# Kernel optimization log

Measured on AMD Instinct MI355X. Metric: run time of the kernel, lower is better.

The kernel has to match this reference:

```python
import jax, jax.numpy as jnp
import numpy as np

N_NODES = 100000
N_EDGES = 1600000
N_GRAPHS = 2000
F_IN = 64
HID = 64


def setup_inputs() -> dict:
    key = jax.random.key(0)
    ks = jax.random.split(key, 8)
    h = jax.random.normal(ks[0], (N_NODES, F_IN), jnp.float32)
    edge_src = jax.random.randint(ks[1], (N_EDGES,), 0, N_NODES, jnp.int32)
    edge_dst = jax.random.randint(ks[2], (N_EDGES,), 0, N_NODES, jnp.int32)
    graph_ids = jnp.sort(jax.random.randint(ks[3], (N_NODES,), 0, N_GRAPHS, jnp.int32))
    # GraphConv weights (glorot-ish scale) and biases, 3 layers 64->64
    sc = 1.0 / np.sqrt(F_IN)
    W0 = jax.random.normal(ks[4], (F_IN, HID), jnp.float32) * sc
    W1 = jax.random.normal(ks[5], (HID, HID), jnp.float32) * sc
    W2 = jax.random.normal(ks[6], (HID, HID), jnp.float32) * sc
    b0 = jnp.zeros((HID,), jnp.float32)
    b1 = jnp.zeros((HID,), jnp.float32)
    b2 = jnp.zeros((HID,), jnp.float32)
    return dict(h=h, edge_src=edge_src, edge_dst=edge_dst, graph_ids=graph_ids,
                W0=W0, b0=b0, W1=W1, b1=b1, W2=W2, b2=b2)


def _gcn_layer(h, W, b, src, dst, out_deg_isqrt, in_deg_isqrt, apply_relu):
    # DGL GraphConv, norm='both': D_in^{-1/2} A D_out^{-1/2} h W + b
    hw = (h * out_deg_isqrt[:, None]) @ W          # weight/norm commute with sum
    m = jax.ops.segment_sum(hw[src], dst, num_segments=N_NODES)  # gather->scatter-add
    m = m * in_deg_isqrt[:, None] + b
    return jax.nn.relu(m) if apply_relu else m


def reference(h, edge_src, edge_dst, graph_ids, W0, b0, W1, b1, W2, b2):
    ones = jnp.ones((N_EDGES,), h.dtype)
    out_deg = jnp.clip(jax.ops.segment_sum(ones, edge_src, num_segments=N_NODES), 1.0, None)
    in_deg = jnp.clip(jax.ops.segment_sum(ones, edge_dst, num_segments=N_NODES), 1.0, None)
    odi = jax.lax.rsqrt(out_deg)
    idi = jax.lax.rsqrt(in_deg)
    params = [(W0, b0), (W1, b1), (W2, b2)]
    for i, (W, b) in enumerate(params):
        h = _gcn_layer(h, W, b, edge_src, edge_dst, odi, idi, apply_relu=(i < len(params) - 1))
    # self.factor = sqrt(dim) / mean(||h||) computed as python float -> detached constant
    factor = jnp.sqrt(jnp.asarray(HID, h.dtype)) / jnp.mean(jnp.linalg.norm(h, axis=1))
    factor = jax.lax.stop_gradient(factor)
    h = h * factor
    # SumPooling over batched graphs
    return jax.ops.segment_sum(h, graph_ids, num_segments=N_GRAPHS)
```

## Files before the change

### kernel.cpp

```cpp
#include <hip/hip_runtime.h>
#include <hip/hip_fp16.h>

#define N_NODES 100000
#define N_EDGES 1600000
#define N_GRAPHS 2000
#define HID 64
#define NB 391
#define CH 4096
#define CAP 5120
#define GATHER_GRID 2048
#define GEMM_GRID 512
#define N_GROUPS (N_NODES / 4)
#define N_TILE16 (N_NODES / 16)

typedef _Float16 half8 __attribute__((ext_vector_type(8)));
typedef float f32x4 __attribute__((ext_vector_type(4)));

__global__ __launch_bounds__(256) void k_zero_i32(int* __restrict__ p, int n) {
    int i = blockIdx.x * 256 + threadIdx.x;
    if (i < n) p[i] = 0;
}

__global__ __launch_bounds__(256) void k_partition_dual(const int* __restrict__ src, const int* __restrict__ dst,
                                                        int* __restrict__ gcur_dst, int* __restrict__ gcur_src,
                                                        unsigned* __restrict__ part_dst,
                                                        unsigned char* __restrict__ part_src) {
    __shared__ unsigned stage[CH];
    __shared__ int lcnt[NB];
    __shared__ int lexcl[NB];
    __shared__ int lofs[NB];
    __shared__ int runbase[NB];
    __shared__ int scanbuf[512];
    int tid = threadIdx.x;
    int e0 = blockIdx.x * CH;
    int n = min(CH, N_EDGES - e0);

    int sv[16], dv[16];
#pragma unroll
    for (int k = 0; k < 16; ++k) {
        int i = k * 256 + tid;
        if (i < n) { sv[k] = src[e0 + i]; dv[k] = dst[e0 + i]; }
        else dv[k] = -1;
    }

    for (int i = tid; i < NB; i += 256) lcnt[i] = 0;
    __syncthreads();
#pragma unroll
    for (int k = 0; k < 16; ++k)
        if (dv[k] >= 0) atomicAdd(&lcnt[dv[k] >> 8], 1);
    __syncthreads();
    for (int s = tid; s < 512; s += 256) scanbuf[s] = (s < NB) ? lcnt[s] : 0;
    __syncthreads();
    for (int off = 1; off < 512; off <<= 1) {
        int i0 = tid, i1 = tid + 256;
        int v0 = scanbuf[i0] + ((i0 >= off) ? scanbuf[i0 - off] : 0);
        int v1 = scanbuf[i1] + ((i1 >= off) ? scanbuf[i1 - off] : 0);
        __syncthreads();
        scanbuf[i0] = v0;
        scanbuf[i1] = v1;
        __syncthreads();
    }
    for (int i = tid; i < NB; i += 256) {
        int ex = scanbuf[i] - lcnt[i];
        lexcl[i] = ex;
        lofs[i] = ex;
    }
    __syncthreads();
#pragma unroll
    for (int k = 0; k < 16; ++k) {
        if (dv[k] >= 0) {
            int p = atomicAdd(&lofs[dv[k] >> 8], 1);
            stage[p] = ((unsigned)sv[k] << 8) | (unsigned)(dv[k] & 255);
        }
    }
    __syncthreads();
    for (int b = tid; b < NB; b += 256)
        if (lcnt[b]) runbase[b] = atomicAdd(&gcur_dst[b], lcnt[b]);
    __syncthreads();
    for (int i = tid; i < n; i += 256) {
        int lo = 0, hi = NB - 1;
        while (lo < hi) {
            int mid = (lo + hi + 1) >> 1;
            if (lexcl[mid] <= i) lo = mid; else hi = mid - 1;
        }
        int pos = runbase[lo] + (i - lexcl[lo]);
        if (pos < CAP) part_dst[(size_t)lo * CAP + pos] = stage[i];
    }
    __syncthreads();

    for (int i = tid; i < NB; i += 256) lcnt[i] = 0;
    __syncthreads();
#pragma unroll
    for (int k = 0; k < 16; ++k)
        if (dv[k] >= 0) atomicAdd(&lcnt[sv[k] >> 8], 1);
    __syncthreads();
    for (int s = tid; s < 512; s += 256) scanbuf[s] = (s < NB) ? lcnt[s] : 0;
    __syncthreads();
    for (int off = 1; off < 512; off <<= 1) {
        int i0 = tid, i1 = tid + 256;
        int v0 = scanbuf[i0] + ((i0 >= off) ? scanbuf[i0 - off] : 0);
        int v1 = scanbuf[i1] + ((i1 >= off) ? scanbuf[i1 - off] : 0);
        __syncthreads();
        scanbuf[i0] = v0;
        scanbuf[i1] = v1;
        __syncthreads();
    }
    for (int i = tid; i < NB; i += 256) {
        int ex = scanbuf[i] - lcnt[i];
        lexcl[i] = ex;
        lofs[i] = ex;
    }
    __syncthreads();
    unsigned char* stage8 = (unsigned char*)stage;
#pragma unroll
    for (int k = 0; k < 16; ++k) {
        if (dv[k] >= 0) {
            int p = atomicAdd(&lofs[sv[k] >> 8], 1);
            stage8[p] = (unsigned char)(sv[k] & 255);
        }
    }
    __syncthreads();
    for (int b = tid; b < NB; b += 256)
        if (lcnt[b]) runbase[b] = atomicAdd(&gcur_src[b], lcnt[b]);
    __syncthreads();
    for (int i = tid; i < n; i += 256) {
        int lo = 0, hi = NB - 1;
        while (lo < hi) {
            int mid = (lo + hi + 1) >> 1;
            if (lexcl[mid] <= i) lo = mid; else hi = mid - 1;
        }
        int pos = runbase[lo] + (i - lexcl[lo]);
        if (pos < CAP) part_src[(size_t)lo * CAP + pos] = stage8[i];
    }
}

__global__ __launch_bounds__(512) void k_scan_buckets(const int* __restrict__ gcur_dst,
                                                      int* __restrict__ bucket_base) {
    __shared__ int sd[512];
    int tid = threadIdx.x;
    int v = (tid < NB) ? gcur_dst[tid] : 0;
    sd[tid] = v;
    __syncthreads();
    for (int off = 1; off < 512; off <<= 1) {
        int t = (tid >= off) ? sd[tid - off] : 0;
        __syncthreads();
        sd[tid] += t;
        __syncthreads();
    }
    if (tid < NB) bucket_base[tid] = sd[tid] - v;
    if (tid == 0) bucket_base[NB] = sd[NB - 1];
}

__global__ __launch_bounds__(256) void k_csr(const unsigned* __restrict__ part_dst,
                                             const int* __restrict__ bucket_base,
                                             int* __restrict__ rowbeg, int* __restrict__ rowend,
                                             float* __restrict__ idi, int* __restrict__ col) {
    __shared__ int cnt[256];
    __shared__ int cur[256];
    __shared__ int wsum[4];
    int b = blockIdx.x;
    int tid = threadIdx.x;
    int base = bucket_base[b];
    int nE = bucket_base[b + 1] - base;
    const unsigned* pb = part_dst + (size_t)b * CAP;
    cnt[tid] = 0;
    __syncthreads();
    for (int i = tid; i < nE; i += 256) atomicAdd(&cnt[pb[i] & 255], 1);
    __syncthreads();
    int c = cnt[tid];
    int incl = c;
#pragma unroll
    for (int off = 1; off < 64; off <<= 1) {
        int t = __shfl_up(incl, off, 64);
        if ((tid & 63) >= off) incl += t;
    }
    if ((tid & 63) == 63) wsum[tid >> 6] = incl;
    __syncthreads();
    int add = 0;
    for (int w = 0; w < (tid >> 6); ++w) add += wsum[w];
    incl += add;
    int excl = incl - c;
    int v = b * 256 + tid;
    if (v < N_NODES) {
        rowbeg[v] = base + excl;
        rowend[v] = base + incl;
        idi[v] = rsqrtf((float)max(c, 1));
    }
    cur[tid] = excl;
    __syncthreads();
    for (int i = tid; i < nE; i += 256) {
        unsigned e = pb[i];
        int p = atomicAdd(&cur[e & 255], 1);
        col[base + p] = (int)(e >> 8);
    }
}

__global__ __launch_bounds__(256) void k_count(const unsigned char* __restrict__ part_src,
                                               const int* __restrict__ gcur_src,
                                               float* __restrict__ odi) {
    __shared__ int cnt[256];
    int b = blockIdx.x;
    int tid = threadIdx.x;
    int nE = gcur_src[b];
    const unsigned char* pb = part_src + (size_t)b * CAP;
    cnt[tid] = 0;
    __syncthreads();
    for (int i = tid; i < nE; i += 256) atomicAdd(&cnt[pb[i]], 1);
    __syncthreads();
    int v = b * 256 + tid;
    if (v < N_NODES) odi[v] = rsqrtf((float)max(cnt[tid], 1));
}

template <int F32IN>
__global__ __launch_bounds__(256) void k_gemm_mfma(const void* __restrict__ inv,
                                                   const float* __restrict__ W,
                                                   const float* __restrict__ odi,
                                                   __half* __restrict__ zs) {
    __shared__ _Float16 Wt[64 * 64];
    int tid = threadIdx.x;
    for (int i = tid; i < 4096; i += 256) {
        int k = i >> 6, j = i & 63;
        Wt[j * 64 + k] = (_Float16)W[i];
    }
    __syncthreads();

    int lane = tid & 63;
    int wid = tid >> 6;
    int lrow = lane & 15;
    int lgrp = lane >> 4;

    half8 Bf[4][2];
#pragma unroll
    for (int nt = 0; nt < 4; ++nt)
#pragma unroll
        for (int kh = 0; kh < 2; ++kh)
            Bf[nt][kh] = *(half8*)&Wt[(nt * 16 + lrow) * 64 + kh * 32 + lgrp * 8];

    for (int t = blockIdx.x * 4 + wid; t < N_TILE16; t += GEMM_GRID * 4) {
        int v0 = t * 16;
        half8 a0, a1;
        if (F32IN) {
            const float* A = (const float*)inv + (size_t)(v0 + lrow) * 64 + lgrp * 8;
            float4 f0 = *(const float4*)A;
            float4 f1 = *(const float4*)(A + 4);
            float4 g0 = *(const float4*)(A + 32);
            float4 g1 = *(const float4*)(A + 36);
            a0[0] = (_Float16)f0.x; a0[1] = (_Float16)f0.y; a0[2] = (_Float16)f0.z; a0[3] = (_Float16)f0.w;
            a0[4] = (_Float16)f1.x; a0[5] = (_Float16)f1.y; a0[6] = (_Float16)f1.z; a0[7] = (_Float16)f1.w;
            a1[0] = (_Float16)g0.x; a1[1] = (_Float16)g0.y; a1[2] = (_Float16)g0.z; a1[3] = (_Float16)g0.w;
            a1[4] = (_Float16)g1.x; a1[5] = (_Float16)g1.y; a1[6] = (_Float16)g1.z; a1[7] = (_Float16)g1.w;
        } else {
            const _Float16* A = (const _Float16*)inv + (size_t)(v0 + lrow) * 64 + lgrp * 8;
            a0 = *(const half8*)A;
            a1 = *(const half8*)(A + 32);
        }
        f32x4 acc[4];
#pragma unroll
        for (int nt = 0; nt < 4; ++nt) { acc[nt] = (f32x4)0.f; }
#pragma unroll
        for (int nt = 0; nt < 4; ++nt) {
            acc[nt] = __builtin_amdgcn_mfma_f32_16x16x32_f16(a0, Bf[nt][0], acc[nt], 0, 0, 0);
            acc[nt] = __builtin_amdgcn_mfma_f32_16x16x32_f16(a1, Bf[nt][1], acc[nt], 0, 0, 0);
        }
#pragma unroll
        for (int r = 0; r < 4; ++r) {
            int node = v0 + lgrp * 4 + r;
            float w = odi[node];
#pragma unroll
            for (int nt = 0; nt < 4; ++nt)
                zs[(size_t)node * 64 + nt * 16 + lrow] = __float2half_rn(acc[nt][r] * w);
        }
    }
}

template <int RELU, int LAST>
__global__ __launch_bounds__(256) void k_gather(const __half* __restrict__ zs, const int* __restrict__ rowbeg,
                                                const int* __restrict__ rowend, const int* __restrict__ col,
                                                const float* __restrict__ idi, const float* __restrict__ b,
                                                __half* __restrict__ xout, float* __restrict__ outF,
                                                float* __restrict__ partials) {
    __shared__ float part[4];
    int tid = threadIdx.x;
    int lane = tid & 63;
    int wid = tid >> 6;
    float bias = b[lane];
    float nacc = 0.f;

    for (int g = blockIdx.x; g < N_GROUPS; g += GATHER_GRID) {
        int v = __builtin_amdgcn_readfirstlane(g * 4 + wid);
        int beg = rowbeg[v], end = rowend[v];
        float a0 = 0.f, a1 = 0.f, a2 = 0.f, a3 = 0.f;
        int p = beg;
        for (; p + 8 <= end; p += 8) {
            int s0 = col[p + 0], s1 = col[p + 1], s2 = col[p + 2], s3 = col[p + 3];
            int s4 = col[p + 4], s5 = col[p + 5], s6 = col[p + 6], s7 = col[p + 7];
            a0 += __half2float(zs[s0 * 64 + lane]);
            a1 += __half2float(zs[s1 * 64 + lane]);
            a2 += __half2float(zs[s2 * 64 + lane]);
            a3 += __half2float(zs[s3 * 64 + lane]);
            a0 += __half2float(zs[s4 * 64 + lane]);
            a1 += __half2float(zs[s5 * 64 + lane]);
            a2 += __half2float(zs[s6 * 64 + lane]);
            a3 += __half2float(zs[s7 * 64 + lane]);
        }
        if (p < end) {
#pragma unroll
            for (int k = 0; k < 8; ++k) {
                int q = (p + k < end) ? (p + k) : (end - 1);
                float xv = __half2float(zs[col[q] * 64 + lane]);
                xv = (p + k < end) ? xv : 0.f;
                if (k & 2) { if (k & 1) a3 += xv; else a2 += xv; }
                else       { if (k & 1) a1 += xv; else a0 += xv; }
            }
        }
        float o = fmaf(((a0 + a1) + (a2 + a3)), idi[v], bias);
        if (RELU) o = fmaxf(o, 0.f);

        if (LAST) {
            outF[(size_t)v * 64 + lane] = o;
            float s = o * o;
#pragma unroll
            for (int off = 32; off > 0; off >>= 1) s += __shfl_xor(s, off, 64);
            if (lane == 0) nacc += sqrtf(s);
        } else {
            xout[(size_t)v * 64 + lane] = __float2half_rn(o);
        }
    }

    if (LAST) {
        if (lane == 0) part[wid] = nacc;
        __syncthreads();
        if (tid == 0) partials[blockIdx.x] = part[0] + part[1] + part[2] + part[3];
    }
}

__global__ __launch_bounds__(256) void k_reduce_factor(const float* __restrict__ partials,
                                                       float* __restrict__ factor) {
    __shared__ float sd[256];
    int tid = threadIdx.x;
    float s = 0.f;
    for (int i = tid; i < GATHER_GRID; i += 256) s += partials[i];
    sd[tid] = s;
    __syncthreads();
    for (int off = 128; off > 0; off >>= 1) {
        if (tid < off) sd[tid] += sd[tid + off];
        __syncthreads();
    }
    if (tid == 0) factor[0] = 8.0f * (float)N_NODES / sd[0];
}

#define POOL_CHUNK 32
__global__ __launch_bounds__(256) void k_pool(const float* __restrict__ h, const int* __restrict__ gid,
                                              const float* __restrict__ factor, float* __restrict__ out) {
    int wave = (blockIdx.x * 256 + threadIdx.x) >> 6;
    int lane = threadIdx.x & 63;
    int v0 = wave * POOL_CHUNK;
    if (v0 >= N_NODES) return;
    float f = factor[0];
    int vend = min(v0 + POOL_CHUNK, N_NODES);
    int gprev = gid[v0];
    float acc = 0.f;
    for (int v = v0; v < vend; ++v) {
        int g = gid[v];
        if (g != gprev) {
            atomicAdd(&out[(size_t)gprev * 64 + lane], acc);
            acc = 0.f;
            gprev = g;
        }
        acc = fmaf(h[(size_t)v * 64 + lane], f, acc);
    }
    atomicAdd(&out[(size_t)gprev * 64 + lane], acc);
}

extern "C" void kernel_launch(void* const* d_in, const int* in_sizes, int n_in,
                              void* d_out, int out_size, void* d_ws, size_t ws_size,
                              hipStream_t stream) {
    const float* h    = (const float*)d_in[0];
    const int*   esrc = (const int*)d_in[1];
    const int*   edst = (const int*)d_in[2];
    const int*   gids = (const int*)d_in[3];
    const float* W0 = (const float*)d_in[4];
    const float* b0 = (const float*)d_in[5];
    const float* W1 = (const float*)d_in[6];
    const float* b1 = (const float*)d_in[7];
    const float* W2 = (const float*)d_in[8];
    const float* b2 = (const float*)d_in[9];
    float* out = (float*)d_out;

    char* wsp = (char*)d_ws;
    size_t off = 0;
    auto alloc = [&](size_t bytes) -> void* {
        void* p = wsp + off;
        off += (bytes + 255) & ~(size_t)255;
        return p;
    };
    int*   gcur       = (int*)alloc((size_t)(2 * NB) * 4);
    int*   bucket_base= (int*)alloc((size_t)(NB + 1) * 4);
    float* odi        = (float*)alloc((size_t)N_NODES * 4);
    float* idi        = (float*)alloc((size_t)N_NODES * 4);
    int*   rowbeg     = (int*)alloc((size_t)N_NODES * 4);
    int*   rowend     = (int*)alloc((size_t)N_NODES * 4);
    float* partials   = (float*)alloc((size_t)GATHER_GRID * 4);
    float* factor     = (float*)alloc(4);
    int*   col        = (int*)alloc((size_t)N_EDGES * 4);
    __half* zsb       = (__half*)alloc((size_t)N_NODES * 64 * 2);
    __half* xh        = (__half*)alloc((size_t)N_NODES * 64 * 2);
    float* outF       = (float*)alloc((size_t)N_NODES * 64 * 4);
    unsigned*      part_dst = (unsigned*)outF;
    unsigned char* part_src = (unsigned char*)outF + (size_t)NB * CAP * 4;

    int* gcur_dst = gcur;
    int* gcur_src = gcur + NB;

    k_zero_i32<<<(2 * NB + 255) / 256, 256, 0, stream>>>(gcur, 2 * NB);
    k_zero_i32<<<(N_GRAPHS * 64 + 255) / 256, 256, 0, stream>>>((int*)out, N_GRAPHS * 64);

    int nchunks = (N_EDGES + CH - 1) / CH;
    k_partition_dual<<<nchunks, 256, 0, stream>>>(esrc, edst, gcur_dst, gcur_src, part_dst, part_src);
    k_scan_buckets<<<1, 512, 0, stream>>>(gcur_dst, bucket_base);
    k_csr<<<NB, 256, 0, stream>>>(part_dst, bucket_base, rowbeg, rowend, idi, col);
    k_count<<<NB, 256, 0, stream>>>(part_src, gcur_src, odi);

    k_gemm_mfma<1><<<GEMM_GRID, 256, 0, stream>>>(h, W0, odi, zsb);
    k_gather<1, 0><<<GATHER_GRID, 256, 0, stream>>>(zsb, rowbeg, rowend, col, idi, b0, xh, nullptr, nullptr);
    k_gemm_mfma<0><<<GEMM_GRID, 256, 0, stream>>>(xh, W1, odi, zsb);
    k_gather<1, 0><<<GATHER_GRID, 256, 0, stream>>>(zsb, rowbeg, rowend, col, idi, b1, xh, nullptr, nullptr);
    k_gemm_mfma<0><<<GEMM_GRID, 256, 0, stream>>>(xh, W2, odi, zsb);
    k_gather<0, 1><<<GATHER_GRID, 256, 0, stream>>>(zsb, rowbeg, rowend, col, idi, b2, nullptr, outF, partials);

    k_reduce_factor<<<1, 256, 0, stream>>>(partials, factor);
    int poolWaves  = (N_NODES + POOL_CHUNK - 1) / POOL_CHUNK;
    int poolBlocks = (poolWaves + 3) / 4;
    k_pool<<<poolBlocks, 256, 0, stream>>>(outF, gids, factor, out);
}
```

Measured before the change: 241.1 us.

## Halve partition chunk, store bucket ids in LDS, merge CSR and count kernels

Halves the edge chunk per partition block so twice as many blocks run, raising occupancy and parallelism during partitioning. Each block now records every staged edge's bucket id in a shared-memory array, replacing the per-element binary search over bucket offsets during scatter. The CSR build and out-degree count kernels are merged into one launch with twice the blocks, saving a launch and letting both run concurrently. The cost is more global atomics on the bucket cursors and smaller, less coalesced runs per bucket.

```diff
diff --git a/kernel.cpp b/kernel.cpp
--- a/kernel.cpp
+++ b/kernel.cpp
@@ -6,7 +6,7 @@
 #define N_GRAPHS 2000
 #define HID 64
 #define NB 391
-#define CH 4096
+#define CH 2048
 #define CAP 5120
 #define GATHER_GRID 2048
 #define GEMM_GRID 512
@@ -26,6 +26,7 @@
                                                         unsigned* __restrict__ part_dst,
                                                         unsigned char* __restrict__ part_src) {
     __shared__ unsigned stage[CH];
+    __shared__ unsigned short stageB[CH];
     __shared__ int lcnt[NB];
     __shared__ int lexcl[NB];
     __shared__ int lofs[NB];
@@ -35,9 +36,9 @@
     int e0 = blockIdx.x * CH;
     int n = min(CH, N_EDGES - e0);
 
-    int sv[16], dv[16];
-#pragma unroll
-    for (int k = 0; k < 16; ++k) {
+    int sv[8], dv[8];
+#pragma unroll
+    for (int k = 0; k < 8; ++k) {
         int i = k * 256 + tid;
         if (i < n) { sv[k] = src[e0 + i]; dv[k] = dst[e0 + i]; }
         else dv[k] = -1;
@@ -46,7 +47,7 @@
     for (int i = tid; i < NB; i += 256) lcnt[i] = 0;
     __syncthreads();
 #pragma unroll
-    for (int k = 0; k < 16; ++k)
+    for (int k = 0; k < 8; ++k)
         if (dv[k] >= 0) atomicAdd(&lcnt[dv[k] >> 8], 1);
     __syncthreads();
     for (int s = tid; s < 512; s += 256) scanbuf[s] = (s < NB) ? lcnt[s] : 0;
@@ -67,10 +68,12 @@
     }
     __syncthreads();
 #pragma unroll
-    for (int k = 0; k < 16; ++k) {
+    for (int k = 0; k < 8; ++k) {
         if (dv[k] >= 0) {
-            int p = atomicAdd(&lofs[dv[k] >> 8], 1);
+            int b = dv[k] >> 8;
+            int p = atomicAdd(&lofs[b], 1);
             stage[p] = ((unsigned)sv[k] << 8) | (unsigned)(dv[k] & 255);
+            stageB[p] = (unsigned short)b;
         }
     }
     __syncthreads();
@@ -78,20 +81,16 @@
         if (lcnt[b]) runbase[b] = atomicAdd(&gcur_dst[b], lcnt[b]);
     __syncthreads();
     for (int i = tid; i < n; i += 256) {
-        int lo = 0, hi = NB - 1;
-        while (lo < hi) {
-            int mid = (lo + hi + 1) >> 1;
-            if (lexcl[mid] <= i) lo = mid; else hi = mid - 1;
-        }
-        int pos = runbase[lo] + (i - lexcl[lo]);
-        if (pos < CAP) part_dst[(size_t)lo * CAP + pos] = stage[i];
+        int b = stageB[i];
+        int pos = runbase[b] + (i - lexcl[b]);
+        if (pos < CAP) part_dst[(size_t)b * CAP + pos] = stage[i];
     }
     __syncthreads();
 
     for (int i = tid; i < NB; i += 256) lcnt[i] = 0;
     __syncthreads();
 #pragma unroll
-    for (int k = 0; k < 16; ++k)
+    for (int k = 0; k < 8; ++k)
         if (dv[k] >= 0) atomicAdd(&lcnt[sv[k] >> 8], 1);
     __syncthreads();
     for (int s = tid; s < 512; s += 256) scanbuf[s] = (s < NB) ? lcnt[s] : 0;
@@ -113,10 +112,12 @@
     __syncthreads();
     unsigned char* stage8 = (unsigned char*)stage;
 #pragma unroll
-    for (int k = 0; k < 16; ++k) {
+    for (int k = 0; k < 8; ++k) {
         if (dv[k] >= 0) {
-            int p = atomicAdd(&lofs[sv[k] >> 8], 1);
+            int b = sv[k] >> 8;
+            int p = atomicAdd(&lofs[b], 1);
             stage8[p] = (unsigned char)(sv[k] & 255);
+            stageB[p] = (unsigned short)b;
         }
     }
     __syncthreads();
@@ -124,13 +125,9 @@
         if (lcnt[b]) runbase[b] = atomicAdd(&gcur_src[b], lcnt[b]);
     __syncthreads();
     for (int i = tid; i < n; i += 256) {
-        int lo = 0, hi = NB - 1;
-        while (lo < hi) {
-            int mid = (lo + hi + 1) >> 1;
-            if (lexcl[mid] <= i) lo = mid; else hi = mid - 1;
-        }
-        int pos = runbase[lo] + (i - lexcl[lo]);
-        if (pos < CAP) part_src[(size_t)lo * CAP + pos] = stage8[i];
+        int b = stageB[i];
+        int pos = runbase[b] + (i - lexcl[b]);
+        if (pos < CAP) part_src[(size_t)b * CAP + pos] = stage8[i];
     }
 }
 
@@ -151,15 +148,30 @@
     if (tid == 0) bucket_base[NB] = sd[NB - 1];
 }
 
-__global__ __launch_bounds__(256) void k_csr(const unsigned* __restrict__ part_dst,
-                                             const int* __restrict__ bucket_base,
-                                             int* __restrict__ rowbeg, int* __restrict__ rowend,
-                                             float* __restrict__ idi, int* __restrict__ col) {
+__global__ __launch_bounds__(256) void k_csr_count(const unsigned* __restrict__ part_dst,
+                                                   const unsigned char* __restrict__ part_src,
+                                                   const int* __restrict__ bucket_base,
+                                                   const int* __restrict__ gcur_src,
+                                                   int* __restrict__ rowbeg, int* __restrict__ rowend,
+                                                   float* __restrict__ idi, float* __restrict__ odi,
+                                                   int* __restrict__ col) {
     __shared__ int cnt[256];
     __shared__ int cur[256];
     __shared__ int wsum[4];
+    int tid = threadIdx.x;
+    if (blockIdx.x >= NB) {
+        int b = blockIdx.x - NB;
+        int nE = gcur_src[b];
+        const unsigned char* pb = part_src + (size_t)b * CAP;
+        cnt[tid] = 0;
+        __syncthreads();
+        for (int i = tid; i < nE; i += 256) atomicAdd(&cnt[pb[i]], 1);
+        __syncthreads();
+        int v = b * 256 + tid;
+        if (v < N_NODES) odi[v] = rsqrtf((float)max(cnt[tid], 1));
+        return;
+    }
     int b = blockIdx.x;
-    int tid = threadIdx.x;
     int base = bucket_base[b];
     int nE = bucket_base[b + 1] - base;
     const unsigned* pb = part_dst + (size_t)b * CAP;
@@ -193,22 +205,6 @@
         int p = atomicAdd(&cur[e & 255], 1);
         col[base + p] = (int)(e >> 8);
     }
-}
-
-__global__ __launch_bounds__(256) void k_count(const unsigned char* __restrict__ part_src,
-                                               const int* __restrict__ gcur_src,
-                                               float* __restrict__ odi) {
-    __shared__ int cnt[256];
-    int b = blockIdx.x;
-    int tid = threadIdx.x;
-    int nE = gcur_src[b];
-    const unsigned char* pb = part_src + (size_t)b * CAP;
-    cnt[tid] = 0;
-    __syncthreads();
-    for (int i = tid; i < nE; i += 256) atomicAdd(&cnt[pb[i]], 1);
-    __syncthreads();
-    int v = b * 256 + tid;
-    if (v < N_NODES) odi[v] = rsqrtf((float)max(cnt[tid], 1));
 }
 
 template <int F32IN>
@@ -418,8 +414,8 @@
     int nchunks = (N_EDGES + CH - 1) / CH;
     k_partition_dual<<<nchunks, 256, 0, stream>>>(esrc, edst, gcur_dst, gcur_src, part_dst, part_src);
     k_scan_buckets<<<1, 512, 0, stream>>>(gcur_dst, bucket_base);
-    k_csr<<<NB, 256, 0, stream>>>(part_dst, bucket_base, rowbeg, rowend, idi, col);
-    k_count<<<NB, 256, 0, stream>>>(part_src, gcur_src, odi);
+    k_csr_count<<<2 * NB, 256, 0, stream>>>(part_dst, part_src, bucket_base, gcur_src,
+                                            rowbeg, rowend, idi, odi, col);
 
     k_gemm_mfma<1><<<GEMM_GRID, 256, 0, stream>>>(h, W0, odi, zsb);
     k_gather<1, 0><<<GATHER_GRID, 256, 0, stream>>>(zsb, rowbeg, rowend, col, idi, b0, xh, nullptr, nullptr);
```

Result: no change. 239.0 us (-0.9%).
